# Optimization experiments

Measured on AMD Instinct MI355X. Metric: run time of the kernel, lower is better.

## Reference

```python
import jax, jax.numpy as jnp
import numpy as np


def _gcn_norm(edge_index, num_nodes):
    # PyG GCNConv default: add self-loops, symmetric deg^{-1/2} normalization.
    loops = jnp.arange(num_nodes, dtype=edge_index.dtype)
    row = jnp.concatenate([edge_index[0], loops])  # source nodes
    col = jnp.concatenate([edge_index[1], loops])  # target nodes (aggregation)
    deg = jax.ops.segment_sum(jnp.ones_like(col, dtype=jnp.float32), col,
                              num_segments=num_nodes)
    dinv = jnp.where(deg > 0, jax.lax.rsqrt(jnp.maximum(deg, 1.0)), 0.0)
    norm = dinv[row] * dinv[col]  # [E + N]
    return row, col, norm


def _gcn_conv(x, row, col, norm, W, b, num_nodes):
    h = x @ W                                   # [N, F_out] linear first (F_out small)
    msg = norm[:, None] * h[row]                # gather + scale  [E+N, F_out]
    out = jax.ops.segment_sum(msg, col, num_segments=num_nodes)  # scatter-add
    return out + b


def setup_inputs() -> dict:
    key = jax.random.key(0)
    k1, k2, k3, k4, k5, k6, k7 = jax.random.split(key, 7)
    N, E, G = 100000, 3200000, 1024
    in_dim, hidden_dim, out_dim = 2, 32, 32
    x = jax.random.normal(k1, (N, in_dim), dtype=jnp.float32)
    edge_index = jax.random.randint(k2, (2, E), 0, N, dtype=jnp.int64)
    batch = jnp.sort(jax.random.randint(k3, (N,), 0, G, dtype=jnp.int64))
    W1 = jax.random.normal(k4, (in_dim, hidden_dim), dtype=jnp.float32) / np.sqrt(in_dim)
    b1 = jnp.zeros((hidden_dim,), dtype=jnp.float32)
    W2 = jax.random.normal(k5, (hidden_dim, out_dim), dtype=jnp.float32) / np.sqrt(hidden_dim)
    b2 = jnp.zeros((out_dim,), dtype=jnp.float32)
    return {"x": x, "edge_index": edge_index, "batch": batch,
            "num_graphs": G, "W1": W1, "b1": b1, "W2": W2, "b2": b2}


def reference(x, edge_index, batch, num_graphs, W1, b1, W2, b2):
    N = x.shape[0]
    row, col, norm = _gcn_norm(edge_index, N)  # shared across both layers
    h = jax.nn.relu(_gcn_conv(x, row, col, norm, W1, b1, N))
    h = _gcn_conv(h, row, col, norm, W2, b2, N)
    # global_mean_pool over `batch`
    sums = jax.ops.segment_sum(h, batch, num_segments=num_graphs)
    cnts = jax.ops.segment_sum(jnp.ones((N,), dtype=h.dtype), batch,
                               num_segments=num_graphs)
    return sums / jnp.maximum(cnts, 1.0)[:, None]
```

## Files before the change

kernel.cpp:

```cpp
#include <hip/hip_runtime.h>

#define FDIM 32
#define BSHIFT 8
#define CPB (1 << BSHIFT)
#define CMASK (CPB - 1)
#define PAD 16
#define MAXBUK 512
#define BNT 4096
#define LCAP 12288

__global__ void k_zero(int* __restrict__ bcur, float* __restrict__ pool, int nb, int np) {
    int i = blockIdx.x * blockDim.x + threadIdx.x;
    if (i < nb) bcur[i] = 0;
    if (i < np) pool[i] = 0.0f;
}

__global__ void k_binsort(const int* __restrict__ row, const int* __restrict__ col,
                          int* bcur, unsigned int* __restrict__ buf, int E, int cap, int NBUK) {
    __shared__ unsigned int lh[MAXBUK];
    __shared__ int lbase[MAXBUK];
    __shared__ int gbase[MAXBUK];
    __shared__ unsigned int swave[4];
    __shared__ unsigned int lpair[BNT];
    int t = threadIdx.x;
    int w = t >> 6, lane = t & 63;
    int base = blockIdx.x * BNT;
    int end = min(base + BNT, E);

    lh[t] = 0u; lh[t + 256] = 0u;
    __syncthreads();

    int cl[16], rw[16];
    #pragma unroll
    for (int k = 0; k < 4; ++k) {
        int e4 = (base >> 2) + k * 256 + t;
        int eb = 4 * e4;
        if (eb + 3 < end) {
            int4 c4 = *(const int4*)(col + eb);
            int4 r4 = *(const int4*)(row + eb);
            cl[4*k] = c4.x; cl[4*k+1] = c4.y; cl[4*k+2] = c4.z; cl[4*k+3] = c4.w;
            rw[4*k] = r4.x; rw[4*k+1] = r4.y; rw[4*k+2] = r4.z; rw[4*k+3] = r4.w;
            atomicAdd(&lh[c4.x >> BSHIFT], 1u);
            atomicAdd(&lh[c4.y >> BSHIFT], 1u);
            atomicAdd(&lh[c4.z >> BSHIFT], 1u);
            atomicAdd(&lh[c4.w >> BSHIFT], 1u);
        } else {
            #pragma unroll
            for (int q = 0; q < 4; ++q) {
                int e = eb + q;
                if (e < end) {
                    cl[4*k+q] = col[e];
                    rw[4*k+q] = row[e];
                    atomicAdd(&lh[cl[4*k+q] >> BSHIFT], 1u);
                } else cl[4*k+q] = -1;
            }
        }
    }
    __syncthreads();

    int i0 = w * 128 + lane * 2;
    unsigned int a = lh[i0], b = lh[i0 + 1];
    unsigned int sum = a + b;
    unsigned int sc = sum;
    #pragma unroll
    for (int off = 1; off < 64; off <<= 1) {
        unsigned int u = __shfl_up(sc, off);
        if (lane >= off) sc += u;
    }
    if (lane == 63) swave[w] = sc;
    __syncthreads();
    unsigned int woff = 0;
    for (int k = 0; k < w; ++k) woff += swave[k];
    lbase[i0]     = (int)(woff + sc - sum);
    lbase[i0 + 1] = (int)(woff + sc - sum + a);
    __syncthreads();

    for (int bb = t; bb < NBUK; bb += 256) {
        unsigned int c = lh[bb];
        int g = bb * cap + (c ? atomicAdd(&bcur[bb * PAD], (int)c) : 0);
        gbase[bb] = g;
        lh[bb] = (unsigned int)g;
    }
    __syncthreads();

    #pragma unroll
    for (int k = 0; k < 16; ++k) {
        if (cl[k] >= 0) {
            int bb = cl[k] >> BSHIFT;
            int gpos = (int)atomicAdd(&lh[bb], 1u);
            int lslot = gpos - gbase[bb] + lbase[bb];
            lpair[lslot] = ((unsigned int)(cl[k] & CMASK) << 24) | (unsigned int)rw[k];
        }
    }
    __syncthreads();

    int tilesz = end - base;
    for (int j = t; j < tilesz; j += 256) {
        int pos = 0;
        #pragma unroll
        for (int step = 256; step; step >>= 1) {
            int np = pos + step;
            if (np < MAXBUK && lbase[np] <= j) pos = np;
        }
        buf[gbase[pos] + (j - lbase[pos])] = lpair[j];
    }
}

__global__ void k_csort(unsigned int* __restrict__ buf, const int* __restrict__ bcur,
                        int* __restrict__ row_ptr, unsigned int* __restrict__ count,
                        const float* __restrict__ x, float* __restrict__ dinv,
                        float2* __restrict__ y, float4* __restrict__ triple,
                        int cap, int N) {
    __shared__ unsigned int lp[LCAP];
    __shared__ unsigned int lh[CPB];
    __shared__ int lofs[CPB];
    __shared__ unsigned int swave[4];
    int b = blockIdx.x;
    int t = threadIdx.x;
    int w = t >> 6, lane = t & 63;
    int c0 = b << BSHIFT;
    int s = b * cap;
    int cntb = bcur[b * PAD];
    lh[t] = 0u;
    if (b == 0 && t == 0) {
        y[N] = make_float2(0.0f, 0.0f);
        triple[N] = make_float4(0.0f, 0.0f, 0.0f, 0.0f);
    }
    __syncthreads();
    for (int j = t; j < cntb; j += 256) {
        unsigned int u = buf[s + j];
        lp[j] = u;
        atomicAdd(&lh[u >> 24], 1u);
    }
    __syncthreads();
    unsigned int v = lh[t];
    unsigned int pv = (v + 7u) & ~7u;
    unsigned int sc = pv;
    #pragma unroll
    for (int off = 1; off < 64; off <<= 1) {
        unsigned int u = __shfl_up(sc, off);
        if (lane >= off) sc += u;
    }
    if (lane == 63) swave[w] = sc;
    __syncthreads();
    unsigned int woff = 0;
    for (int k = 0; k < w; ++k) woff += swave[k];
    int excl = s + (int)(woff + sc - pv);
    int c = c0 + t;
    if (c < N) {
        row_ptr[c] = excl;
        count[c] = v;
        float dv = rsqrtf((float)v + 1.0f);
        dinv[c] = dv;
        float2 xv = ((const float2*)x)[c];
        y[c] = make_float2(dv * xv.x, dv * xv.y);
    }
    lofs[t] = excl;
    __syncthreads();
    for (int j = t; j < cntb; j += 256) {
        unsigned int u = lp[j];
        int pos = atomicAdd(&lofs[u >> 24], 1);
        buf[pos] = u & 0x00FFFFFFu;
    }
    for (unsigned int k = v; k < pv; ++k) buf[excl + k] = (unsigned int)N;
}


__global__ void k_prep(const float* __restrict__ x, const unsigned int* __restrict__ count,
                       float* __restrict__ dinv, float2* __restrict__ y,
                       float4* __restrict__ triple, int N) {
    int i = blockIdx.x * blockDim.x + threadIdx.x;
    if (i == 0) {
        y[N] = make_float2(0.0f, 0.0f);
        triple[N] = make_float4(0.0f, 0.0f, 0.0f, 0.0f);
    }
    if (i >= N) return;
    float dv = rsqrtf((float)count[i] + 1.0f);
    dinv[i] = dv;
    float2 xv = ((const float2*)x)[i];
    y[i] = make_float2(dv * xv.x, dv * xv.y);
}

__global__ void k_agg1(const int* __restrict__ row_ptr, const unsigned int* __restrict__ count,
                       const int* __restrict__ sorted_row, const float2* __restrict__ y,
                       const float* __restrict__ dinv, float4* __restrict__ triple, int N) {
    int t = threadIdx.x;
    int i = blockIdx.x * 32 + (t >> 3), l = t & 7;
    if (i >= N) return;
    int s = row_ptr[i];
    int e = s + (int)count[i];
    float zx = 0.0f, zy = 0.0f;
    for (int j = s + l; j < e; j += 8) {
        float2 yv = y[sorted_row[j]];
        zx += yv.x; zy += yv.y;
    }
    #pragma unroll
    for (int m = 4; m >= 1; m >>= 1) {
        zx += __shfl_xor(zx, m);
        zy += __shfl_xor(zy, m);
    }
    if (l == 0) {
        float2 yi = y[i];
        zx += yi.x; zy += yi.y;
        float dv = dinv[i];
        triple[i] = make_float4(dv * zx, dv * zy, dv, 0.0f);
    }
}

__device__ __forceinline__ float4 f4fma(float s, float4 m, float4 a) {
    return make_float4(fmaf(s, m.x, a.x), fmaf(s, m.y, a.y),
                       fmaf(s, m.z, a.z), fmaf(s, m.w, a.w));
}
__device__ __forceinline__ float4 f4relu(float4 q) {
    return make_float4(fmaxf(q.x, 0.f), fmaxf(q.y, 0.f), fmaxf(q.z, 0.f), fmaxf(q.w, 0.f));
}

__global__ void __launch_bounds__(256)
k_agg_pool(const int* __restrict__ row_ptr, const unsigned int* __restrict__ count,
           const int* __restrict__ sorted_row, const float4* __restrict__ triple,
           const float* __restrict__ W1, const float* __restrict__ b1,
           const int* __restrict__ batch, float* __restrict__ pool,
           float* __restrict__ cnt, int N) {
    __shared__ float sh[32][FDIM];
    __shared__ int sb[32];
    int t = threadIdx.x;
    int n = t >> 3, l = t & 7;
    int i = blockIdx.x * 32 + n;
    int fa = 4 * l;
    float4 w0 = *(const float4*)(W1 + fa);
    float4 w1 = *(const float4*)(W1 + FDIM + fa);
    float4 bb = *(const float4*)(b1 + fa);
    float4 acc = make_float4(0.f, 0.f, 0.f, 0.f);
    int bt = -1;
    if (i < N) {
        float4 ts = triple[i];
        float dv = ts.z;
        acc = f4fma(ts.z, f4relu(f4fma(ts.x, w0, f4fma(ts.y, w1, bb))), acc);
        int s = row_ptr[i];
        int pv = ((int)count[i] + 7) & ~7;
        for (int j = s; j < s + pv; j += 8) {
            int4 ra = *(const int4*)(sorted_row + j);
            int4 rb = *(const int4*)(sorted_row + j + 4);
            float4 t0 = triple[ra.x], t1 = triple[ra.y], t2 = triple[ra.z], t3 = triple[ra.w];
            float4 t4 = triple[rb.x], t5 = triple[rb.y], t6 = triple[rb.z], t7 = triple[rb.w];
            acc = f4fma(t0.z, f4relu(f4fma(t0.x, w0, f4fma(t0.y, w1, bb))), acc);
            acc = f4fma(t1.z, f4relu(f4fma(t1.x, w0, f4fma(t1.y, w1, bb))), acc);
            acc = f4fma(t2.z, f4relu(f4fma(t2.x, w0, f4fma(t2.y, w1, bb))), acc);
            acc = f4fma(t3.z, f4relu(f4fma(t3.x, w0, f4fma(t3.y, w1, bb))), acc);
            acc = f4fma(t4.z, f4relu(f4fma(t4.x, w0, f4fma(t4.y, w1, bb))), acc);
            acc = f4fma(t5.z, f4relu(f4fma(t5.x, w0, f4fma(t5.y, w1, bb))), acc);
            acc = f4fma(t6.z, f4relu(f4fma(t6.x, w0, f4fma(t6.y, w1, bb))), acc);
            acc = f4fma(t7.z, f4relu(f4fma(t7.x, w0, f4fma(t7.y, w1, bb))), acc);
        }
        acc.x *= dv; acc.y *= dv; acc.z *= dv; acc.w *= dv;
        bt = batch[i];
    }
    *(float4*)&sh[n][fa] = acc;
    if (l == 0) sb[n] = bt;
    __syncthreads();
    if (bt >= 0 && (n == 0 || sb[n - 1] != bt)) {
        float4 ssum = acc;
        int m = n + 1;
        for (; m < 32 && sb[m] == bt; ++m) {
            float4 o = *(const float4*)&sh[m][fa];
            ssum.x += o.x; ssum.y += o.y; ssum.z += o.z; ssum.w += o.w;
        }
        atomicAdd(&pool[bt * FDIM + fa],     ssum.x);
        atomicAdd(&pool[bt * FDIM + fa + 1], ssum.y);
        atomicAdd(&pool[bt * FDIM + fa + 2], ssum.z);
        atomicAdd(&pool[bt * FDIM + fa + 3], ssum.w);
        if (l == 0) atomicAdd(&cnt[bt], (float)(m - n));
    }
}

__global__ void k_out(const float* __restrict__ pool, const float* __restrict__ cnt,
                      const float* __restrict__ W2, const float* __restrict__ b2,
                      float* __restrict__ out, int G) {
    __shared__ float sW[FDIM * FDIM];
    int t = threadIdx.x;
    for (int k = t; k < FDIM * FDIM; k += 256) sW[k] = W2[k];
    __syncthreads();
    int g = blockIdx.x * 8 + (t >> 5), f = t & 31;
    if (g >= G) return;
    float c = cnt[g];
    float o = 0.0f;
    if (c > 0.0f) {
        float s = 0.0f;
        #pragma unroll
        for (int k = 0; k < FDIM; ++k) s = fmaf(pool[g * FDIM + k], sW[k * FDIM + f], s);
        o = fmaf(s, 1.0f / c, b2[f]);
    }
    out[g * FDIM + f] = o;
}


__global__ void k_fhist(const int* __restrict__ col, unsigned int* __restrict__ count, int E) {
    int i = blockIdx.x * blockDim.x + threadIdx.x;
    if (i < E) atomicAdd(&count[col[i]], 1u);
}
__global__ void k_fsc2(const int* __restrict__ row, const int* __restrict__ col,
                       const float2* __restrict__ y, float* __restrict__ z, int E) {
    int e = blockIdx.x * blockDim.x + threadIdx.x;
    if (e >= E) return;
    float2 yv = y[row[e]];
    int c = col[e];
    atomicAdd(&z[2 * c],     yv.x);
    atomicAdd(&z[2 * c + 1], yv.y);
}
__global__ void k_fmkt(const float* __restrict__ z, const float2* __restrict__ y,
                       const float* __restrict__ dinv, float4* __restrict__ triple, int N) {
    int i = blockIdx.x * blockDim.x + threadIdx.x;
    if (i >= N) return;
    float dv = dinv[i];
    float2 yi = y[i];
    triple[i] = make_float4(dv * (z[2 * i] + yi.x), dv * (z[2 * i + 1] + yi.y), dv, 0.0f);
}
__global__ void k_fsc32(const int* __restrict__ row, const int* __restrict__ col,
                        const float4* __restrict__ triple, const float* __restrict__ W1,
                        const float* __restrict__ b1, float* __restrict__ v, int total) {
    int idx = blockIdx.x * blockDim.x + threadIdx.x;
    if (idx >= total) return;
    int e = idx >> 5, f = idx & 31;
    float4 tr = triple[row[e]];
    float u = tr.z * fmaxf(fmaf(tr.x, W1[f], fmaf(tr.y, W1[FDIM + f], b1[f])), 0.0f);
    atomicAdd(&v[col[e] * FDIM + f], u);
}
__global__ void k_ffin(const float4* __restrict__ triple, const float* __restrict__ v,
                       const float* __restrict__ W1, const float* __restrict__ b1,
                       const int* __restrict__ batch, float* __restrict__ pool,
                       float* __restrict__ cnt, int N) {
    int idx = blockIdx.x * blockDim.x + threadIdx.x;
    int i = idx >> 5, f = idx & 31;
    if (i >= N) return;
    float4 tr = triple[i];
    float u = tr.z * fmaxf(fmaf(tr.x, W1[f], fmaf(tr.y, W1[FDIM + f], b1[f])), 0.0f);
    float w = tr.z * (u + v[i * FDIM + f]);
    int b = batch[i];
    atomicAdd(&pool[b * FDIM + f], w);
    if (f == 0) atomicAdd(&cnt[b], 1.0f);
}

extern "C" void kernel_launch(void* const* d_in, const int* in_sizes, int n_in,
                              void* d_out, int out_size, void* d_ws, size_t ws_size,
                              hipStream_t stream) {
    const float* x   = (const float*)d_in[0];
    const int*   ei  = (const int*)d_in[1];
    const int* batch = (const int*)d_in[2];
    const float* W1  = (const float*)d_in[4];
    const float* b1  = (const float*)d_in[5];
    const float* W2  = (const float*)d_in[6];
    const float* b2  = (const float*)d_in[7];
    float* out = (float*)d_out;

    int N = in_sizes[0] / 2;
    int E = in_sizes[1] / 2;
    int G = out_size / FDIM;

    const int* row = ei;
    const int* col = ei + E;

    int NB = (N + 255) / 256;
    int NBUK = (N + CMASK) >> BSHIFT;

    int capBase = (E + NBUK - 1) / NBUK;
    int cap = capBase + capBase / 8 + 2048;
    cap = (cap + 7) & ~7;

    size_t off = 0;
    size_t o_bcur = off;  off += (size_t)NBUK * PAD;
    size_t o_cnt  = off;  off += N;
    size_t o_rp   = off;  off += N;
    size_t o_dv   = off;  off += N;
    size_t o_y    = off;  off += 2ull * (N + 1);
    off = (off + 3) & ~(size_t)3;
    size_t o_tr   = off;  off += 4ull * (N + 1);
    size_t o_buf  = off;  off += (size_t)NBUK * cap;
    size_t o_pool = off;  off += 32ull * G;
    size_t o_cg   = off;  off += G;
    size_t elemsNew = off;

    unsigned int* W = (unsigned int*)d_ws;

    if (ws_size >= elemsNew * 4 && N < (1 << 24) && NBUK <= MAXBUK && cap <= LCAP) {
        int* bcur           = (int*)(W + o_bcur);
        unsigned int* count = (unsigned int*)(W + o_cnt);
        int* row_ptr        = (int*)(W + o_rp);
        float* dinv         = (float*)(W + o_dv);
        float2* y           = (float2*)(W + o_y);
        float4* triple      = (float4*)(W + o_tr);
        unsigned int* buf   = W + o_buf;
        float* pool         = (float*)(W + o_pool);
        float* cntg         = (float*)(W + o_cg);

        int nb = NBUK * PAD;
        int np = G * FDIM + G;
        int zgrid = (max(nb, np) + 255) / 256;
        k_zero<<<zgrid, 256, 0, stream>>>(bcur, pool, nb, np);

        k_binsort<<<(E + BNT - 1) / BNT, 256, 0, stream>>>(row, col, bcur, buf, E, cap, NBUK);
        k_csort<<<NBUK, 256, 0, stream>>>(buf, bcur, row_ptr, count, x, dinv, y, triple, cap, N);

        k_agg1<<<(N + 31) / 32, 256, 0, stream>>>(row_ptr, count, (const int*)buf, y, dinv,
                                                  triple, N);
        k_agg_pool<<<(N + 31) / 32, 256, 0, stream>>>(row_ptr, count, (const int*)buf, triple,
                                                      W1, b1, batch, pool, cntg, N);
        k_out<<<(G + 7) / 8, 256, 0, stream>>>(pool, cntg, W2, b2, out, G);
    } else {
        unsigned int* count = (unsigned int*)d_ws;
        float* dinv         = (float*)(count + N);
        float2* y           = (float2*)(dinv + N);
        float* z            = (float*)(y + N + 1);
        size_t toff = ((size_t)(z + 2 * N - (float*)d_ws) + 3) & ~(size_t)3;
        float4* triple      = (float4*)((float*)d_ws + toff);
        float* v            = (float*)(triple + N + 1);
        float* pool         = v + 32ull * N;
        float* cntg         = pool + 32ull * G;

        hipMemsetAsync(count, 0, (size_t)N * 4, stream);
        hipMemsetAsync(z, 0, (size_t)N * 8, stream);
        hipMemsetAsync(v, 0, (size_t)N * FDIM * 4, stream);
        hipMemsetAsync(pool, 0, (size_t)(G * FDIM + G) * 4, stream);

        k_fhist<<<(E + 255) / 256, 256, 0, stream>>>(col, count, E);
        k_prep<<<NB, 256, 0, stream>>>(x, count, dinv, y, triple, N);
        k_fsc2<<<(E + 255) / 256, 256, 0, stream>>>(row, col, y, z, E);
        k_fmkt<<<NB, 256, 0, stream>>>(z, y, dinv, triple, N);
        int ts = E * FDIM;
        k_fsc32<<<(ts + 255) / 256, 256, 0, stream>>>(row, col, triple, W1, b1, v, ts);
        k_ffin<<<(N * FDIM + 255) / 256, 256, 0, stream>>>(triple, v, W1, b1, batch, pool, cntg, N);
        k_out<<<(G + 7) / 8, 256, 0, stream>>>(pool, cntg, W2, b2, out, G);
    }
}
```

Measured before the change: 133.9 us.

## Pad per-tile bucket chunks to 16 with sentinels and double binsort tile size

The bin-sort kernel now processes 8192 edges per block with 512 threads. Each block reserves bucket space in multiples of 16 entries and fills the unused slots with a sentinel, so global writes land on aligned segments and there are fewer bucket atomics per edge. The column-sort kernel skips sentinel entries, and bucket capacity is recomputed to absorb the per-tile padding. In exchange, the bucket buffer grows and the second kernel reads and tests the extra padded slots.

```diff
diff --git a/kernel.cpp b/kernel.cpp
--- a/kernel.cpp
+++ b/kernel.cpp
@@ -6,8 +6,10 @@
 #define CMASK (CPB - 1)
 #define PAD 16
 #define MAXBUK 512
-#define BNT 4096
+#define BNT 8192
+#define BTHREADS 512
 #define LCAP 12288
+#define SENT 0xFFFFFFFFu
 
 __global__ void k_zero(int* __restrict__ bcur, float* __restrict__ pool, int nb, int np) {
     int i = blockIdx.x * blockDim.x + threadIdx.x;
@@ -15,8 +17,9 @@
     if (i < np) pool[i] = 0.0f;
 }
 
-__global__ void k_binsort(const int* __restrict__ row, const int* __restrict__ col,
-                          int* bcur, unsigned int* __restrict__ buf, int E, int cap, int NBUK) {
+__global__ void __launch_bounds__(BTHREADS)
+k_binsort(const int* __restrict__ row, const int* __restrict__ col,
+          int* bcur, unsigned int* __restrict__ buf, int E, int cap, int NBUK) {
     __shared__ unsigned int lh[MAXBUK];
     __shared__ int lbase[MAXBUK];
     __shared__ int gbase[MAXBUK];
@@ -26,14 +29,15 @@
     int w = t >> 6, lane = t & 63;
     int base = blockIdx.x * BNT;
     int end = min(base + BNT, E);
-
-    lh[t] = 0u; lh[t + 256] = 0u;
+    int tilesz = end - base;
+
+    if (t < MAXBUK) lh[t] = 0u;
     __syncthreads();
 
     int cl[16], rw[16];
     #pragma unroll
     for (int k = 0; k < 4; ++k) {
-        int e4 = (base >> 2) + k * 256 + t;
+        int e4 = (base >> 2) + k * BTHREADS + t;
         int eb = 4 * e4;
         if (eb + 3 < end) {
             int4 c4 = *(const int4*)(col + eb);
@@ -58,26 +62,31 @@
     }
     __syncthreads();
 
-    int i0 = w * 128 + lane * 2;
-    unsigned int a = lh[i0], b = lh[i0 + 1];
-    unsigned int sum = a + b;
-    unsigned int sc = sum;
-    #pragma unroll
-    for (int off = 1; off < 64; off <<= 1) {
-        unsigned int u = __shfl_up(sc, off);
-        if (lane >= off) sc += u;
-    }
-    if (lane == 63) swave[w] = sc;
-    __syncthreads();
-    unsigned int woff = 0;
-    for (int k = 0; k < w; ++k) woff += swave[k];
-    lbase[i0]     = (int)(woff + sc - sum);
-    lbase[i0 + 1] = (int)(woff + sc - sum + a);
-    __syncthreads();
-
-    for (int bb = t; bb < NBUK; bb += 256) {
+    if (w < 4) {
+        int i0 = w * 128 + lane * 2;
+        unsigned int a = lh[i0], b = lh[i0 + 1];
+        unsigned int sum = a + b;
+        unsigned int sc = sum;
+        #pragma unroll
+        for (int off = 1; off < 64; off <<= 1) {
+            unsigned int u = __shfl_up(sc, off);
+            if (lane >= off) sc += u;
+        }
+        if (lane == 63) swave[w] = sc;
+        __syncthreads();
+        unsigned int woff = 0;
+        for (int k = 0; k < w; ++k) woff += swave[k];
+        lbase[i0]     = (int)(woff + sc - sum);
+        lbase[i0 + 1] = (int)(woff + sc - sum + a);
+    } else {
+        __syncthreads();
+    }
+    __syncthreads();
+
+    for (int bb = t; bb < NBUK; bb += BTHREADS) {
         unsigned int c = lh[bb];
-        int g = bb * cap + (c ? atomicAdd(&bcur[bb * PAD], (int)c) : 0);
+        unsigned int cp = (c + 15u) & ~15u;
+        int g = bb * cap + (cp ? atomicAdd(&bcur[bb * PAD], (int)cp) : 0);
         gbase[bb] = g;
         lh[bb] = (unsigned int)g;
     }
@@ -94,8 +103,7 @@
     }
     __syncthreads();
 
-    int tilesz = end - base;
-    for (int j = t; j < tilesz; j += 256) {
+    for (int j = t; j < tilesz; j += BTHREADS) {
         int pos = 0;
         #pragma unroll
         for (int step = 256; step; step >>= 1) {
@@ -103,6 +111,15 @@
             if (np < MAXBUK && lbase[np] <= j) pos = np;
         }
         buf[gbase[pos] + (j - lbase[pos])] = lpair[j];
+    }
+
+    for (int bb = t; bb < NBUK; bb += BTHREADS) {
+        int lb = lbase[bb];
+        int cend = (bb + 1 < NBUK) ? lbase[bb + 1] : tilesz;
+        int c = cend - lb;
+        int cp = (c + 15) & ~15;
+        int g = gbase[bb];
+        for (int k = c; k < cp; ++k) buf[g + k] = SENT;
     }
 }
 
@@ -130,7 +147,7 @@
     for (int j = t; j < cntb; j += 256) {
         unsigned int u = buf[s + j];
         lp[j] = u;
-        atomicAdd(&lh[u >> 24], 1u);
+        if (u != SENT) atomicAdd(&lh[u >> 24], 1u);
     }
     __syncthreads();
     unsigned int v = lh[t];
@@ -159,8 +176,10 @@
     __syncthreads();
     for (int j = t; j < cntb; j += 256) {
         unsigned int u = lp[j];
-        int pos = atomicAdd(&lofs[u >> 24], 1);
-        buf[pos] = u & 0x00FFFFFFu;
+        if (u != SENT) {
+            int pos = atomicAdd(&lofs[u >> 24], 1);
+            buf[pos] = u & 0x00FFFFFFu;
+        }
     }
     for (unsigned int k = v; k < pv; ++k) buf[excl + k] = (unsigned int)N;
 }
@@ -361,10 +380,11 @@
 
     int NB = (N + 255) / 256;
     int NBUK = (N + CMASK) >> BSHIFT;
+    int ntiles = (E + BNT - 1) / BNT;
 
     int capBase = (E + NBUK - 1) / NBUK;
-    int cap = capBase + capBase / 8 + 2048;
-    cap = (cap + 7) & ~7;
+    int cap = capBase + ntiles * 8 + 512;
+    cap = (cap + 15) & ~15;
 
     size_t off = 0;
     size_t o_bcur = off;  off += (size_t)NBUK * PAD;
@@ -397,7 +417,7 @@
         int zgrid = (max(nb, np) + 255) / 256;
         k_zero<<<zgrid, 256, 0, stream>>>(bcur, pool, nb, np);
 
-        k_binsort<<<(E + BNT - 1) / BNT, 256, 0, stream>>>(row, col, bcur, buf, E, cap, NBUK);
+        k_binsort<<<ntiles, BTHREADS, 0, stream>>>(row, col, bcur, buf, E, cap, NBUK);
         k_csort<<<NBUK, 256, 0, stream>>>(buf, bcur, row_ptr, count, x, dinv, y, triple, cap, N);
 
         k_agg1<<<(N + 31) / 32, 256, 0, stream>>>(row_ptr, count, (const int*)buf, y, dinv,
```

Result: faster. 122.7 us (-8.4%).
